# Performance work log

Measured on AMD Instinct MI355X. Metric: run time of the kernel, lower is better.

Reference implementation:

```python
import jax, jax.numpy as jnp
import numpy as np

NUM_CLASSES = 1000
FEAT_DIM = 2048
BATCH = 16384


def setup_inputs() -> dict:
    key = jax.random.key(0)
    k1, k2 = jax.random.split(key)
    features = jax.random.normal(k1, (BATCH, FEAT_DIM), dtype=jnp.float32)
    labels = jax.random.randint(k2, (BATCH,), 0, NUM_CLASSES, dtype=jnp.int64)
    return {"features": features, "labels": labels}


def _scatters(features, labels):
    # Faithful to the original (note: cosine_dist is 1 - dot/||u|| * ||v||,
    # reproducing the original operator precedence).
    N = features.shape[0]
    C = NUM_CLASSES
    counts = jax.ops.segment_sum(jnp.ones((N,), features.dtype), labels, num_segments=C)  # [C]
    sums = jax.ops.segment_sum(features, labels, num_segments=C)                          # [C, D]
    means = jnp.nan_to_num(sums / counts[:, None])  # per-class means, empty class -> 0
    overall = jnp.mean(features, axis=0)            # [D]

    def cdist(U, v):
        # U: [..., D], v: [D]; matches torch: 1 - dot(u,v)/||u|| * ||v||
        return 1.0 - (U @ v) / jnp.linalg.norm(U, axis=-1) * jnp.linalg.norm(v)

    # St: mean squared cosine-distance of each sample to the overall mean (scalar)
    st = (cdist(features, overall) ** 2).sum() / N

    # Sb (weighted): sum_c Ni/N * dist(mean_c, overall)^2 (scalar)
    d_mb = cdist(means, overall) ** 2                # [C]
    sb = ((counts / N) * d_mb).sum()

    # Sw (weighted): per class, (1/Ni) * sum_{i in c} dist(x_i, mean_c)^2, scaled by Ni/N
    row_mean = means[labels]                         # [N, D]
    d = 1.0 - jnp.einsum('nd,nd->n', features, row_mean) \
        / jnp.linalg.norm(features, axis=-1) * jnp.linalg.norm(row_mean, axis=-1)
    per_class = jax.ops.segment_sum(d ** 2, labels, num_segments=C)  # [C]
    sw_list = (1.0 / counts) * per_class * (counts / N)              # [C]
    return st, sw_list, sb


def reference(features, labels):
    st, sw_list, sb = _scatters(features, labels)
    sw = jnp.mean(sw_list)        # forward: Sw_t = mean(Sw_t, dim=0)
    sb_t = st - sw                # forward: Sb_t = St_t - Sw_t
    return jnp.stack([st, sw, sb_t])
```

## Files before the change

kernel.cpp:

```cpp
#include <hip/hip_runtime.h>
#include <math.h>

#define N_SAMPLES 16384
#define FEAT 2048
#define NCLS 1000
#define CPAD 1024
#define MAXCLS 320
#define NCOLS 256
#define ROWS_PER_COL (N_SAMPLES / NCOLS)


__global__ __launch_bounds__(256) void k1_sort_colsum(
    const int* __restrict__ labels, const float* __restrict__ feat,
    int* __restrict__ counts, int* __restrict__ offsets, int* __restrict__ perm,
    float* __restrict__ part_ov) {
  const int t = threadIdx.x, lane = t & 63, w = t >> 6;
  if (blockIdx.x == 0) {
    __shared__ int h[CPAD];
    __shared__ int cur[CPAD];
    __shared__ int wtot[4];
    for (int i = t; i < CPAD; i += 256) h[i] = 0;
    __syncthreads();
    const int4* lb = (const int4*)labels;
    for (int j = t; j < N_SAMPLES / 4; j += 256) {
      int4 q = lb[j];
      atomicAdd(&h[q.x], 1);
      atomicAdd(&h[q.y], 1);
      atomicAdd(&h[q.z], 1);
      atomicAdd(&h[q.w], 1);
    }
    __syncthreads();
    const int b4 = 4 * t;
    const int e0 = h[b4], e1 = h[b4 + 1], e2 = h[b4 + 2], e3 = h[b4 + 3];
    const int ssum = e0 + e1 + e2 + e3;
    int v = ssum;
    for (int off = 1; off < 64; off <<= 1) {
      int p = __shfl_up(v, off);
      if (lane >= off) v += p;
    }
    if (lane == 63) wtot[w] = v;
    __syncthreads();
    int wb = 0;
    for (int i = 0; i < w; ++i) wb += wtot[i];
    const int excl = wb + v - ssum;
    counts[b4] = e0; counts[b4 + 1] = e1; counts[b4 + 2] = e2; counts[b4 + 3] = e3;
    offsets[b4] = excl;
    offsets[b4 + 1] = excl + e0;
    offsets[b4 + 2] = excl + e0 + e1;
    offsets[b4 + 3] = excl + e0 + e1 + e2;
    cur[b4] = excl;
    cur[b4 + 1] = excl + e0;
    cur[b4 + 2] = excl + e0 + e1;
    cur[b4 + 3] = excl + e0 + e1 + e2;
    __syncthreads();
    for (int j = t; j < N_SAMPLES / 4; j += 256) {
      int4 q = lb[j];
      int idx = 4 * j;
      int p0 = atomicAdd(&cur[q.x], 1); perm[p0] = idx;
      int p1 = atomicAdd(&cur[q.y], 1); perm[p1] = idx + 1;
      int p2 = atomicAdd(&cur[q.z], 1); perm[p2] = idx + 2;
      int p3 = atomicAdd(&cur[q.w], 1); perm[p3] = idx + 3;
    }
  } else {
    const int bb = blockIdx.x - 1;
    const float4* f4 = (const float4*)feat;
    const size_t rowbase = (size_t)bb * ROWS_PER_COL;
    float a0 = 0, a1 = 0, a2 = 0, a3 = 0, b0 = 0, b1 = 0, b2 = 0, b3 = 0;
    for (int r = 0; r < ROWS_PER_COL; r += 4) {
      const float4* p0 = f4 + (rowbase + r) * 512;
      const float4* p1 = f4 + (rowbase + r + 1) * 512;
      const float4* p2 = f4 + (rowbase + r + 2) * 512;
      const float4* p3 = f4 + (rowbase + r + 3) * 512;
      float4 v0 = p0[t], u0 = p0[t + 256];
      float4 v1 = p1[t], u1 = p1[t + 256];
      float4 v2 = p2[t], u2 = p2[t + 256];
      float4 v3 = p3[t], u3 = p3[t + 256];
      a0 += (v0.x + v1.x) + (v2.x + v3.x);
      a1 += (v0.y + v1.y) + (v2.y + v3.y);
      a2 += (v0.z + v1.z) + (v2.z + v3.z);
      a3 += (v0.w + v1.w) + (v2.w + v3.w);
      b0 += (u0.x + u1.x) + (u2.x + u3.x);
      b1 += (u0.y + u1.y) + (u2.y + u3.y);
      b2 += (u0.z + u1.z) + (u2.z + u3.z);
      b3 += (u0.w + u1.w) + (u2.w + u3.w);
    }
    float4* o4 = (float4*)part_ov;
    o4[bb * 512 + t] = make_float4(a0, a1, a2, a3);
    o4[bb * 512 + t + 256] = make_float4(b0, b1, b2, b3);
  }
}

__global__ __launch_bounds__(256) void k2_fold(const float* __restrict__ part_ov,
                                               float* __restrict__ overall) {
  const float4* p4 = (const float4*)part_ov;
  const int t = threadIdx.x;
  const int fi = blockIdx.x * 32 + (t & 31);
  const int g = t >> 5;
  float a0 = 0, a1 = 0, a2 = 0, a3 = 0;
  for (int b = g; b < NCOLS; b += 8) {
    float4 v = p4[b * 512 + fi];
    a0 += v.x; a1 += v.y; a2 += v.z; a3 += v.w;
  }
  __shared__ float4 lds[8][32];
  lds[g][t & 31] = make_float4(a0, a1, a2, a3);
  __syncthreads();
  if (g == 0) {
    float s0 = 0, s1 = 0, s2 = 0, s3 = 0;
#pragma unroll
    for (int i = 0; i < 8; ++i) {
      float4 v = lds[i][t];
      s0 += v.x; s1 += v.y; s2 += v.z; s3 += v.w;
    }
    ((float4*)overall)[fi] = make_float4(s0, s1, s2, s3);
  }
}

__global__ __launch_bounds__(256) void k3_class_pass(
    const float* __restrict__ feat, const int* __restrict__ offsets,
    const int* __restrict__ counts, const int* __restrict__ perm,
    const float* __restrict__ overall, float* __restrict__ pst,
    float* __restrict__ psw) {
  const int c = blockIdx.x, t = threadIdx.x, w = t >> 6, lane = t & 63;
  __shared__ int lperm[MAXCLS];
  __shared__ float sums_lds[FEAT];
  __shared__ float red[4];
  __shared__ float sc[2];
  const int beg = offsets[c], n = counts[c];
  for (int i = t; i < n; i += 256) lperm[i] = perm[beg + i];

  const float4* ov4 = (const float4*)overall;
  {
    float4 o1 = ov4[t], o2 = ov4[t + 256];
    float sq = o1.x * o1.x + o1.y * o1.y + o1.z * o1.z + o1.w * o1.w +
               o2.x * o2.x + o2.y * o2.y + o2.z * o2.z + o2.w * o2.w;
    for (int off = 32; off; off >>= 1) sq += __shfl_xor(sq, off);
    if (lane == 0) red[w] = sq;
    __syncthreads();
    if (t == 0) sc[1] = sqrtf(red[0] + red[1] + red[2] + red[3]);
  }

  const float4* f4 = (const float4*)feat;
  float a0 = 0, a1 = 0, a2 = 0, a3 = 0, b0 = 0, b1 = 0, b2 = 0, b3 = 0;
  int r = 0;
  for (; r + 4 <= n; r += 4) {
    const float4* p0 = f4 + (size_t)lperm[r] * 512;
    const float4* p1 = f4 + (size_t)lperm[r + 1] * 512;
    const float4* p2 = f4 + (size_t)lperm[r + 2] * 512;
    const float4* p3 = f4 + (size_t)lperm[r + 3] * 512;
    float4 v0 = p0[t], u0 = p0[t + 256];
    float4 v1 = p1[t], u1 = p1[t + 256];
    float4 v2 = p2[t], u2 = p2[t + 256];
    float4 v3 = p3[t], u3 = p3[t + 256];
    a0 += (v0.x + v1.x) + (v2.x + v3.x);
    a1 += (v0.y + v1.y) + (v2.y + v3.y);
    a2 += (v0.z + v1.z) + (v2.z + v3.z);
    a3 += (v0.w + v1.w) + (v2.w + v3.w);
    b0 += (u0.x + u1.x) + (u2.x + u3.x);
    b1 += (u0.y + u1.y) + (u2.y + u3.y);
    b2 += (u0.z + u1.z) + (u2.z + u3.z);
    b3 += (u0.w + u1.w) + (u2.w + u3.w);
  }
  for (; r < n; ++r) {
    const float4* p0 = f4 + (size_t)lperm[r] * 512;
    float4 v = p0[t], u = p0[t + 256];
    a0 += v.x; a1 += v.y; a2 += v.z; a3 += v.w;
    b0 += u.x; b1 += u.y; b2 += u.z; b3 += u.w;
  }
  float4* s4 = (float4*)sums_lds;
  s4[t] = make_float4(a0, a1, a2, a3);
  s4[t + 256] = make_float4(b0, b1, b2, b3);
  {
    float sq = a0 * a0 + a1 * a1 + a2 * a2 + a3 * a3 +
               b0 * b0 + b1 * b1 + b2 * b2 + b3 * b3;
    for (int off = 32; off; off >>= 1) sq += __shfl_xor(sq, off);
    __syncthreads();
    if (lane == 0) red[w] = sq;
    __syncthreads();
    if (t == 0) sc[0] = sqrtf(red[0] + red[1] + red[2] + red[3]);
    __syncthreads();
  }

  const float snormv = sc[0], ovn = sc[1];
  const float invN2 = 1.f / ((float)N_SAMPLES * (float)N_SAMPLES);
  const float cnt = (float)n;
  float st_acc = 0.f, sw_acc = 0.f;
  for (int rr = w; rr < n; rr += 4) {
    const float4* xr = f4 + (size_t)lperm[rr] * 512;
    float dxo = 0.f, dxs = 0.f, nx2 = 0.f;
#pragma unroll
    for (int k = 0; k < 8; ++k) {
      float4 x = xr[lane + 64 * k];
      float4 s = s4[lane + 64 * k];
      float4 o = ov4[lane + 64 * k];
      dxo += x.x * o.x + x.y * o.y + x.z * o.z + x.w * o.w;
      dxs += x.x * s.x + x.y * s.y + x.z * s.z + x.w * s.w;
      nx2 += x.x * x.x + x.y * x.y + x.z * x.z + x.w * x.w;
    }
    for (int off = 32; off; off >>= 1) {
      dxo += __shfl_xor(dxo, off);
      dxs += __shfl_xor(dxs, off);
      nx2 += __shfl_xor(nx2, off);
    }
    if (lane == 0) {
      float nx = sqrtf(nx2);
      float t1 = 1.f - dxo * ovn * invN2 / nx;
      float t2 = 1.f - dxs * snormv / (cnt * cnt * nx);
      st_acc += t1 * t1;
      sw_acc += t2 * t2;
    }
  }
  __shared__ float red2[8];
  if (lane == 0) { red2[w] = st_acc; red2[4 + w] = sw_acc; }
  __syncthreads();
  if (t == 0) {
    pst[c] = red2[0] + red2[1] + red2[2] + red2[3];
    psw[c] = red2[4] + red2[5] + red2[6] + red2[7];
  }
}

__global__ __launch_bounds__(256) void k4_final(const float* __restrict__ pst,
                                                const float* __restrict__ psw,
                                                float* __restrict__ out) {
  const int t = threadIdx.x, w = t >> 6, lane = t & 63;
  float st = 0.f, sw = 0.f;
  for (int i = t; i < NCLS; i += 256) { st += pst[i]; sw += psw[i]; }
  for (int off = 32; off; off >>= 1) {
    st += __shfl_xor(st, off);
    sw += __shfl_xor(sw, off);
  }
  __shared__ float rs[4], rw[4];
  if (lane == 0) { rs[w] = st; rw[w] = sw; }
  __syncthreads();
  if (t == 0) {
    float s = rs[0] + rs[1] + rs[2] + rs[3];
    float q = rw[0] + rw[1] + rw[2] + rw[3];
    float stv = s / (float)N_SAMPLES;
    float swv = q / ((float)N_SAMPLES * (float)NCLS);
    out[0] = stv;
    out[1] = swv;
    out[2] = stv - swv;
  }
}

extern "C" void kernel_launch(void* const* d_in, const int* in_sizes, int n_in,
                              void* d_out, int out_size, void* d_ws, size_t ws_size,
                              hipStream_t stream) {
  const float* feat = (const float*)d_in[0];
  const int* labels = (const int*)d_in[1];
  float* out = (float*)d_out;

  float* part_ov = (float*)d_ws;
  float* overall = part_ov + NCOLS * FEAT;
  float* pst = overall + FEAT;
  float* psw = pst + CPAD;
  int* counts = (int*)(psw + CPAD);
  int* offsets = counts + CPAD;
  int* perm = offsets + CPAD;

  k1_sort_colsum<<<NCOLS + 1, 256, 0, stream>>>(labels, feat, counts, offsets, perm,
                                                part_ov);
  k2_fold<<<16, 256, 0, stream>>>(part_ov, overall);
  k3_class_pass<<<NCLS, 256, 0, stream>>>(feat, offsets, counts, perm, overall, pst,
                                          psw);
  k4_final<<<1, 256, 0, stream>>>(pst, psw, out);
}
```

Baseline: 95.33 us.

## Convert features to bf16 in column-sum pass and use bf16 in class pass

The first kernel now writes a bf16 copy of the feature matrix while computing column partial sums, and the class kernel reads that half-size copy twice (class sums and distance pass) instead of fp32 features. Overall mean and class sums are stored as bf16 in LDS, and column blocks are doubled to 512. This aims to cut HBM traffic in the class pass, at the cost of an extra 64MB write in the first pass and reduced precision. MAXCLS drops to 64, which risks overflow if any class has more than 64 samples.

Result: no change. 93.66 us (-1.7%).

```diff
diff --git a/kernel.cpp b/kernel.cpp
--- a/kernel.cpp
+++ b/kernel.cpp
@@ -5,17 +5,52 @@
 #define FEAT 2048
 #define NCLS 1000
 #define CPAD 1024
-#define MAXCLS 320
-#define NCOLS 256
-#define ROWS_PER_COL (N_SAMPLES / NCOLS)
-
-
-__global__ __launch_bounds__(256) void k1_sort_colsum(
-    const int* __restrict__ labels, const float* __restrict__ feat,
-    int* __restrict__ counts, int* __restrict__ offsets, int* __restrict__ perm,
-    float* __restrict__ part_ov) {
+#define COLB 512
+#define ROWS_PER_B (N_SAMPLES / COLB)
+#define MAXCLS 64
+
+
+__device__ __forceinline__ unsigned pack_bf16_2(float lo, float hi) {
+  unsigned ul = __float_as_uint(lo);
+  ul += 0x7FFFu + ((ul >> 16) & 1u);
+  unsigned uh = __float_as_uint(hi);
+  uh += 0x7FFFu + ((uh >> 16) & 1u);
+  return (ul >> 16) | (uh & 0xFFFF0000u);
+}
+__device__ __forceinline__ float bflo(unsigned u) {
+  return __uint_as_float(u << 16);
+}
+__device__ __forceinline__ float bfhi(unsigned u) {
+  return __uint_as_float(u & 0xFFFF0000u);
+}
+
+__global__ __launch_bounds__(256) void k1_col_cvt_sort(
+    const float* __restrict__ feat, const int* __restrict__ labels,
+    unsigned* __restrict__ feat16, float* __restrict__ part_ov,
+    int* __restrict__ counts, int* __restrict__ offsets, int* __restrict__ perm) {
   const int t = threadIdx.x, lane = t & 63, w = t >> 6;
-  if (blockIdx.x == 0) {
+  if (blockIdx.x < COLB) {
+    const int b = blockIdx.x;
+    const float4* f4 = (const float4*)feat;
+    uint2* f16 = (uint2*)feat16;
+    const int base = b * ROWS_PER_B;
+    float a0 = 0, a1 = 0, a2 = 0, a3 = 0, b0 = 0, b1 = 0, b2 = 0, b3 = 0;
+    for (int r = 0; r < ROWS_PER_B; r += 2) {
+      const size_t i0 = (size_t)(base + r) * 512;
+      const size_t i1 = (size_t)(base + r + 1) * 512;
+      float4 v0 = f4[i0 + t], u0 = f4[i0 + 256 + t];
+      float4 v1 = f4[i1 + t], u1 = f4[i1 + 256 + t];
+      f16[i0 + t] = make_uint2(pack_bf16_2(v0.x, v0.y), pack_bf16_2(v0.z, v0.w));
+      f16[i0 + 256 + t] = make_uint2(pack_bf16_2(u0.x, u0.y), pack_bf16_2(u0.z, u0.w));
+      f16[i1 + t] = make_uint2(pack_bf16_2(v1.x, v1.y), pack_bf16_2(v1.z, v1.w));
+      f16[i1 + 256 + t] = make_uint2(pack_bf16_2(u1.x, u1.y), pack_bf16_2(u1.z, u1.w));
+      a0 += v0.x + v1.x; a1 += v0.y + v1.y; a2 += v0.z + v1.z; a3 += v0.w + v1.w;
+      b0 += u0.x + u1.x; b1 += u0.y + u1.y; b2 += u0.z + u1.z; b3 += u0.w + u1.w;
+    }
+    float4* o4 = (float4*)part_ov;
+    o4[(size_t)b * 512 + t] = make_float4(a0, a1, a2, a3);
+    o4[(size_t)b * 512 + 256 + t] = make_float4(b0, b1, b2, b3);
+  } else {
     __shared__ int h[CPAD];
     __shared__ int cur[CPAD];
     __shared__ int wtot[4];
@@ -61,32 +96,6 @@
       int p2 = atomicAdd(&cur[q.z], 1); perm[p2] = idx + 2;
       int p3 = atomicAdd(&cur[q.w], 1); perm[p3] = idx + 3;
     }
-  } else {
-    const int bb = blockIdx.x - 1;
-    const float4* f4 = (const float4*)feat;
-    const size_t rowbase = (size_t)bb * ROWS_PER_COL;
-    float a0 = 0, a1 = 0, a2 = 0, a3 = 0, b0 = 0, b1 = 0, b2 = 0, b3 = 0;
-    for (int r = 0; r < ROWS_PER_COL; r += 4) {
-      const float4* p0 = f4 + (rowbase + r) * 512;
-      const float4* p1 = f4 + (rowbase + r + 1) * 512;
-      const float4* p2 = f4 + (rowbase + r + 2) * 512;
-      const float4* p3 = f4 + (rowbase + r + 3) * 512;
-      float4 v0 = p0[t], u0 = p0[t + 256];
-      float4 v1 = p1[t], u1 = p1[t + 256];
-      float4 v2 = p2[t], u2 = p2[t + 256];
-      float4 v3 = p3[t], u3 = p3[t + 256];
-      a0 += (v0.x + v1.x) + (v2.x + v3.x);
-      a1 += (v0.y + v1.y) + (v2.y + v3.y);
-      a2 += (v0.z + v1.z) + (v2.z + v3.z);
-      a3 += (v0.w + v1.w) + (v2.w + v3.w);
-      b0 += (u0.x + u1.x) + (u2.x + u3.x);
-      b1 += (u0.y + u1.y) + (u2.y + u3.y);
-      b2 += (u0.z + u1.z) + (u2.z + u3.z);
-      b3 += (u0.w + u1.w) + (u2.w + u3.w);
-    }
-    float4* o4 = (float4*)part_ov;
-    o4[bb * 512 + t] = make_float4(a0, a1, a2, a3);
-    o4[bb * 512 + t + 256] = make_float4(b0, b1, b2, b3);
   }
 }
 
@@ -97,8 +106,8 @@
   const int fi = blockIdx.x * 32 + (t & 31);
   const int g = t >> 5;
   float a0 = 0, a1 = 0, a2 = 0, a3 = 0;
-  for (int b = g; b < NCOLS; b += 8) {
-    float4 v = p4[b * 512 + fi];
+  for (int b = g; b < COLB; b += 8) {
+    float4 v = p4[(size_t)b * 512 + fi];
     a0 += v.x; a1 += v.y; a2 += v.z; a3 += v.w;
   }
   __shared__ float4 lds[8][32];
@@ -115,86 +124,86 @@
   }
 }
 
-__global__ __launch_bounds__(256) void k3_class_pass(
-    const float* __restrict__ feat, const int* __restrict__ offsets,
+__global__ __launch_bounds__(256) void k3_class(
+    const unsigned* __restrict__ feat16, const int* __restrict__ offsets,
     const int* __restrict__ counts, const int* __restrict__ perm,
     const float* __restrict__ overall, float* __restrict__ pst,
     float* __restrict__ psw) {
   const int c = blockIdx.x, t = threadIdx.x, w = t >> 6, lane = t & 63;
   __shared__ int lperm[MAXCLS];
-  __shared__ float sums_lds[FEAT];
-  __shared__ float red[4];
-  __shared__ float sc[2];
+  __shared__ uint4 s4lds[256];
+  __shared__ uint4 ovlds[256];
+  __shared__ float red[8];
+  __shared__ float scv;
   const int beg = offsets[c], n = counts[c];
   for (int i = t; i < n; i += 256) lperm[i] = perm[beg + i];
 
-  const float4* ov4 = (const float4*)overall;
-  {
-    float4 o1 = ov4[t], o2 = ov4[t + 256];
-    float sq = o1.x * o1.x + o1.y * o1.y + o1.z * o1.z + o1.w * o1.w +
-               o2.x * o2.x + o2.y * o2.y + o2.z * o2.z + o2.w * o2.w;
-    for (int off = 32; off; off >>= 1) sq += __shfl_xor(sq, off);
-    if (lane == 0) red[w] = sq;
-    __syncthreads();
-    if (t == 0) sc[1] = sqrtf(red[0] + red[1] + red[2] + red[3]);
-  }
-
-  const float4* f4 = (const float4*)feat;
-  float a0 = 0, a1 = 0, a2 = 0, a3 = 0, b0 = 0, b1 = 0, b2 = 0, b3 = 0;
+  const float4* ovf = (const float4*)overall;
+  float4 o1 = ovf[2 * t], o2 = ovf[2 * t + 1];
+  ovlds[t] = make_uint4(pack_bf16_2(o1.x, o1.y), pack_bf16_2(o1.z, o1.w),
+                        pack_bf16_2(o2.x, o2.y), pack_bf16_2(o2.z, o2.w));
+  float sq = o1.x * o1.x + o1.y * o1.y + o1.z * o1.z + o1.w * o1.w +
+             o2.x * o2.x + o2.y * o2.y + o2.z * o2.z + o2.w * o2.w;
+  for (int off = 32; off; off >>= 1) sq += __shfl_xor(sq, off);
+  if (lane == 0) red[w] = sq;
+  __syncthreads();
+  if (t == 0) scv = sqrtf(red[0] + red[1] + red[2] + red[3]);
+  __syncthreads();
+  const float ovn = scv;
+
+  const uint4* fv = (const uint4*)feat16;
+  float S0 = 0, S1 = 0, S2 = 0, S3 = 0, S4 = 0, S5 = 0, S6 = 0, S7 = 0;
+#define ADD8(q)                                            \
+  S0 += bflo(q.x); S1 += bfhi(q.x); S2 += bflo(q.y);       \
+  S3 += bfhi(q.y); S4 += bflo(q.z); S5 += bfhi(q.z);       \
+  S6 += bflo(q.w); S7 += bfhi(q.w);
   int r = 0;
   for (; r + 4 <= n; r += 4) {
-    const float4* p0 = f4 + (size_t)lperm[r] * 512;
-    const float4* p1 = f4 + (size_t)lperm[r + 1] * 512;
-    const float4* p2 = f4 + (size_t)lperm[r + 2] * 512;
-    const float4* p3 = f4 + (size_t)lperm[r + 3] * 512;
-    float4 v0 = p0[t], u0 = p0[t + 256];
-    float4 v1 = p1[t], u1 = p1[t + 256];
-    float4 v2 = p2[t], u2 = p2[t + 256];
-    float4 v3 = p3[t], u3 = p3[t + 256];
-    a0 += (v0.x + v1.x) + (v2.x + v3.x);
-    a1 += (v0.y + v1.y) + (v2.y + v3.y);
-    a2 += (v0.z + v1.z) + (v2.z + v3.z);
-    a3 += (v0.w + v1.w) + (v2.w + v3.w);
-    b0 += (u0.x + u1.x) + (u2.x + u3.x);
-    b1 += (u0.y + u1.y) + (u2.y + u3.y);
-    b2 += (u0.z + u1.z) + (u2.z + u3.z);
-    b3 += (u0.w + u1.w) + (u2.w + u3.w);
+    uint4 q0 = fv[(size_t)lperm[r] * 256 + t];
+    uint4 q1 = fv[(size_t)lperm[r + 1] * 256 + t];
+    uint4 q2 = fv[(size_t)lperm[r + 2] * 256 + t];
+    uint4 q3 = fv[(size_t)lperm[r + 3] * 256 + t];
+    ADD8(q0) ADD8(q1) ADD8(q2) ADD8(q3)
   }
   for (; r < n; ++r) {
-    const float4* p0 = f4 + (size_t)lperm[r] * 512;
-    float4 v = p0[t], u = p0[t + 256];
-    a0 += v.x; a1 += v.y; a2 += v.z; a3 += v.w;
-    b0 += u.x; b1 += u.y; b2 += u.z; b3 += u.w;
-  }
-  float4* s4 = (float4*)sums_lds;
-  s4[t] = make_float4(a0, a1, a2, a3);
-  s4[t + 256] = make_float4(b0, b1, b2, b3);
-  {
-    float sq = a0 * a0 + a1 * a1 + a2 * a2 + a3 * a3 +
-               b0 * b0 + b1 * b1 + b2 * b2 + b3 * b3;
-    for (int off = 32; off; off >>= 1) sq += __shfl_xor(sq, off);
-    __syncthreads();
-    if (lane == 0) red[w] = sq;
-    __syncthreads();
-    if (t == 0) sc[0] = sqrtf(red[0] + red[1] + red[2] + red[3]);
-    __syncthreads();
-  }
-
-  const float snormv = sc[0], ovn = sc[1];
+    uint4 q = fv[(size_t)lperm[r] * 256 + t];
+    ADD8(q)
+  }
+#undef ADD8
+  s4lds[t] = make_uint4(pack_bf16_2(S0, S1), pack_bf16_2(S2, S3),
+                        pack_bf16_2(S4, S5), pack_bf16_2(S6, S7));
+  float sq2 = S0 * S0 + S1 * S1 + S2 * S2 + S3 * S3 +
+              S4 * S4 + S5 * S5 + S6 * S6 + S7 * S7;
+  for (int off = 32; off; off >>= 1) sq2 += __shfl_xor(sq2, off);
+  if (lane == 0) red[w] = sq2;
+  __syncthreads();
+  if (t == 0) scv = sqrtf(red[0] + red[1] + red[2] + red[3]);
+  __syncthreads();
+  const float snormv = scv;
+  const float cnt = (float)n;
   const float invN2 = 1.f / ((float)N_SAMPLES * (float)N_SAMPLES);
-  const float cnt = (float)n;
+
   float st_acc = 0.f, sw_acc = 0.f;
   for (int rr = w; rr < n; rr += 4) {
-    const float4* xr = f4 + (size_t)lperm[rr] * 512;
+    const size_t base = (size_t)lperm[rr] * 256;
     float dxo = 0.f, dxs = 0.f, nx2 = 0.f;
 #pragma unroll
-    for (int k = 0; k < 8; ++k) {
-      float4 x = xr[lane + 64 * k];
-      float4 s = s4[lane + 64 * k];
-      float4 o = ov4[lane + 64 * k];
-      dxo += x.x * o.x + x.y * o.y + x.z * o.z + x.w * o.w;
-      dxs += x.x * s.x + x.y * s.y + x.z * s.z + x.w * s.w;
-      nx2 += x.x * x.x + x.y * x.y + x.z * x.z + x.w * x.w;
+    for (int k = 0; k < 4; ++k) {
+      uint4 x = fv[base + lane + 64 * k];
+      uint4 s = s4lds[lane + 64 * k];
+      uint4 o = ovlds[lane + 64 * k];
+#define DOT2(xw, sw_, ow)                                  \
+  {                                                        \
+    float xl = bflo(xw), xh = bfhi(xw);                    \
+    dxs += xl * bflo(sw_) + xh * bfhi(sw_);                \
+    dxo += xl * bflo(ow) + xh * bfhi(ow);                  \
+    nx2 += xl * xl + xh * xh;                              \
+  }
+      DOT2(x.x, s.x, o.x)
+      DOT2(x.y, s.y, o.y)
+      DOT2(x.z, s.z, o.z)
+      DOT2(x.w, s.w, o.w)
+#undef DOT2
     }
     for (int off = 32; off; off >>= 1) {
       dxo += __shfl_xor(dxo, off);
@@ -249,18 +258,19 @@
   const int* labels = (const int*)d_in[1];
   float* out = (float*)d_out;
 
-  float* part_ov = (float*)d_ws;
-  float* overall = part_ov + NCOLS * FEAT;
+  unsigned* feat16 = (unsigned*)d_ws;
+  float* part_ov = (float*)(feat16 + (size_t)N_SAMPLES * (FEAT / 2));
+  float* overall = part_ov + (size_t)COLB * FEAT;
   float* pst = overall + FEAT;
   float* psw = pst + CPAD;
   int* counts = (int*)(psw + CPAD);
   int* offsets = counts + CPAD;
   int* perm = offsets + CPAD;
 
-  k1_sort_colsum<<<NCOLS + 1, 256, 0, stream>>>(labels, feat, counts, offsets, perm,
-                                                part_ov);
+  k1_col_cvt_sort<<<COLB + 1, 256, 0, stream>>>(feat, labels, feat16, part_ov,
+                                                counts, offsets, perm);
   k2_fold<<<16, 256, 0, stream>>>(part_ov, overall);
-  k3_class_pass<<<NCLS, 256, 0, stream>>>(feat, offsets, counts, perm, overall, pst,
-                                          psw);
+  k3_class<<<NCLS, 256, 0, stream>>>(feat16, offsets, counts, perm, overall, pst,
+                                     psw);
   k4_final<<<1, 256, 0, stream>>>(pst, psw, out);
 }
```
